# Kernel optimization log

Hardware: AMD Instinct MI355X
Metric: run time of the kernel (lower is better)

Reference implementation:

```python
import jax, jax.numpy as jnp
import numpy as np

NUM_CLASSES = 64


def setup_inputs() -> dict:
    key = jax.random.key(0)
    k1, k2, k3, k4, k5 = jax.random.split(key, 5)
    N, D = 65536, 256
    return {
        "src_feat": jax.random.normal(k1, (N, D), dtype=jnp.float32),
        "trg_feat": jax.random.normal(k2, (N, D), dtype=jnp.float32),
        "src_label": jax.random.randint(k3, (N,), 0, NUM_CLASSES, dtype=jnp.int64),
        "trg_label": jax.random.randint(k4, (N,), 0, NUM_CLASSES, dtype=jnp.int64),
        "trg_feat_un": jax.random.normal(k5, (N, D), dtype=jnp.float32),
    }


def _kl_mean(p_logits, q_logits):
    # torch F.kl_div(log_softmax(p), softmax(q), reduction='mean')
    # = mean over ALL elements of q * (log q - log_softmax(p))
    q = jax.nn.softmax(q_logits, axis=-1)
    logq = jax.nn.log_softmax(q_logits, axis=-1)
    logp = jax.nn.log_softmax(p_logits, axis=-1)
    return jnp.mean(q * (logq - logp))


def reference(src_feat, trg_feat, src_label, trg_label, trg_feat_un):
    C = NUM_CLASSES
    ones_s = jnp.ones(src_feat.shape[0], dtype=src_feat.dtype)
    ones_t = jnp.ones(trg_feat.shape[0], dtype=trg_feat.dtype)
    sum_s = jax.ops.segment_sum(src_feat, src_label, num_segments=C)  # [C,D]
    sum_t = jax.ops.segment_sum(trg_feat, trg_label, num_segments=C)  # [C,D]
    cnt_s = jax.ops.segment_sum(ones_s, src_label, num_segments=C)    # [C]
    cnt_t = jax.ops.segment_sum(ones_t, trg_label, num_segments=C)    # [C]
    u_s = sum_s / cnt_s[:, None]
    u_t = sum_t / cnt_t[:, None]
    u_st = (sum_s + sum_t) / (cnt_s + cnt_t)[:, None]

    feats = jnp.concatenate((src_feat, trg_feat), axis=0)  # [2N, D]
    P_s = feats @ u_s.T    # [2N, C]
    P_t = feats @ u_t.T
    P_st = feats @ u_st.T

    loss_st = (_kl_mean(P_s, P_t) + _kl_mean(P_t, P_s)) / 2
    loss_sst = (_kl_mean(P_s, P_st) + _kl_mean(P_st, P_s)) / 2
    loss_tst = (_kl_mean(P_t, P_st) + _kl_mean(P_st, P_t)) / 2
    return (loss_st + loss_sst + loss_tst) / 3
```

## Files before the change

### kernel.cpp

```cpp
#include <hip/hip_runtime.h>

#define N_ROWS 65536
#define DIMS 256
#define NCLS 64

#define P_SUM_S 0
#define P_SUM_T 131072
#define P_CNT_S 262144
#define P_CNT_T 262656
#define F_SUM_S 263168
#define F_SUM_T 279552
#define ACC_OFF 296064
#define BPACK_OFF 296080

typedef __attribute__((ext_vector_type(8))) short bf16x8;
typedef __attribute__((ext_vector_type(4))) float f32x4;

__device__ __forceinline__ short f2bf(float f) {
  unsigned u = __float_as_uint(f);
  u += 0x7fffu + ((u >> 16) & 1u);
  return (short)(u >> 16);
}

__device__ __forceinline__ float wave_sum64(float v) {
#pragma unroll
  for (int m = 32; m > 0; m >>= 1) v += __shfl_xor(v, m, 64);
  return v;
}
__device__ __forceinline__ float seg_max16(float v) {
#pragma unroll
  for (int m = 8; m > 0; m >>= 1) v = fmaxf(v, __shfl_xor(v, m, 64));
  return v;
}
__device__ __forceinline__ float seg_sum16(float v) {
#pragma unroll
  for (int m = 8; m > 0; m >>= 1) v += __shfl_xor(v, m, 64);
  return v;
}

__global__ __launch_bounds__(256) void seg_sum_kernel(
    const float* __restrict__ src_feat, const float* __restrict__ trg_feat,
    const int* __restrict__ src_label, const int* __restrict__ trg_label,
    float* __restrict__ ws_f) {
  __shared__ float lsum[NCLS * DIMS];
  const int tid = threadIdx.x;
  const bool is_trg = blockIdx.x >= 256;
  const int blk = is_trg ? (blockIdx.x - 256) : blockIdx.x;
  const int part = blockIdx.x & 7;
  const float* feat = is_trg ? trg_feat : src_feat;
  const int* label = is_trg ? trg_label : src_label;
  float* gsum = ws_f + (is_trg ? P_SUM_T : P_SUM_S) + part * 16384;
  float* gcnt = ws_f + (is_trg ? P_CNT_T : P_CNT_S) + part * 64;

  for (int i = tid; i < NCLS * DIMS; i += 256) lsum[i] = 0.f;
  __syncthreads();

  const int row0 = blk * 256;
  float cnt_local = 0.f;
  for (int r = 0; r < 256; r += 8) {
    int lb[8];
    float v[8];
#pragma unroll
    for (int i = 0; i < 8; ++i) {
      lb[i] = label[row0 + r + i];
      v[i] = feat[(size_t)(row0 + r + i) * DIMS + tid];
    }
#pragma unroll
    for (int i = 0; i < 8; ++i) {
      lsum[lb[i] * DIMS + tid] += v[i];
      if (tid < NCLS) cnt_local += (lb[i] == tid) ? 1.f : 0.f;
    }
  }
  __syncthreads();
  for (int c = 0; c < NCLS; ++c)
    atomicAdd(&gsum[c * DIMS + tid], lsum[c * DIMS + tid]);
  if (tid < NCLS) atomicAdd(&gcnt[tid], cnt_local);
}

__global__ __launch_bounds__(256) void reduce_kernel(float* __restrict__ ws_f) {
  const int i = blockIdx.x * 256 + threadIdx.x;
  const int which = i >> 14;
  const int off = i & 16383;
  const float* pp = ws_f + (which ? P_SUM_T : P_SUM_S) + off;
  float s = 0.f;
#pragma unroll
  for (int p = 0; p < 8; ++p) s += pp[p * 16384];
  ws_f[(which ? F_SUM_T : F_SUM_S) + off] = s;
}

__global__ __launch_bounds__(64) void pack_kernel(float* __restrict__ ws_f) {
  const int bx = blockIdx.x;
  const int mat = bx >> 2;
  const int tile = bx & 3;
  const int lane = threadIdx.x;
  const int c = tile * 16 + (lane & 15);

  float cs = 0.f, ct = 0.f;
#pragma unroll
  for (int p = 0; p < 8; ++p) {
    cs += ws_f[P_CNT_S + p * 64 + c];
    ct += ws_f[P_CNT_T + p * 64 + c];
  }

  bf16x8* out = (bf16x8*)(ws_f + BPACK_OFF);
  const float* ss_base = ws_f + F_SUM_S + c * DIMS;
  const float* st_base = ws_f + F_SUM_T + c * DIMS;

#pragma unroll
  for (int s = 0; s < 8; ++s) {
    const int k0 = s * 32 + (lane >> 4) * 8;
    bf16x8 v;
#pragma unroll
    for (int j = 0; j < 8; ++j) {
      const float ss = ss_base[k0 + j];
      const float st = st_base[k0 + j];
      float u;
      if (mat == 0) u = ss / cs;
      else if (mat == 1) u = st / ct;
      else u = (ss + st) / (cs + ct);
      v[j] = f2bf(u);
    }
    out[(bx * 8 + s) * 64 + lane] = v;
  }
}

__global__ __launch_bounds__(256, 2) void main_kernel(
    const float* __restrict__ src_feat, const float* __restrict__ trg_feat,
    const float* __restrict__ ws_f, double* __restrict__ acc_out) {
  const int tid = threadIdx.x;
  const int wave = tid >> 6;
  const int lane = tid & 63;
  const int row0 = blockIdx.x * 128 + wave * 32;
  const float* base = (row0 < N_ROWS)
                          ? src_feat + (size_t)row0 * DIMS
                          : trg_feat + (size_t)(row0 - N_ROWS) * DIMS;
  const float* ap = base + (size_t)((lane & 15) * DIMS + (lane >> 4) * 8);
  const bf16x8* bp = (const bf16x8*)(ws_f + BPACK_OFF);

  f32x4 C[3][4][2];
#pragma unroll
  for (int m = 0; m < 3; ++m)
#pragma unroll
    for (int t = 0; t < 4; ++t)
#pragma unroll
      for (int g = 0; g < 2; ++g) C[m][t][g] = (f32x4){0.f, 0.f, 0.f, 0.f};

#pragma unroll
  for (int s = 0; s < 8; ++s) {
    bf16x8 a[2];
#pragma unroll
    for (int g = 0; g < 2; ++g) {
      const float* p = ap + g * 16 * DIMS + s * 32;
      const float4 lo = *(const float4*)p;
      const float4 hi = *(const float4*)(p + 4);
      bf16x8 t;
      t[0] = f2bf(lo.x); t[1] = f2bf(lo.y); t[2] = f2bf(lo.z); t[3] = f2bf(lo.w);
      t[4] = f2bf(hi.x); t[5] = f2bf(hi.y); t[6] = f2bf(hi.z); t[7] = f2bf(hi.w);
      a[g] = t;
    }
#pragma unroll
    for (int mt = 0; mt < 12; ++mt) {
      const bf16x8 b = bp[(mt * 8 + s) * 64 + lane];
      C[mt >> 2][mt & 3][0] =
          __builtin_amdgcn_mfma_f32_16x16x32_bf16(a[0], b, C[mt >> 2][mt & 3][0], 0, 0, 0);
      C[mt >> 2][mt & 3][1] =
          __builtin_amdgcn_mfma_f32_16x16x32_bf16(a[1], b, C[mt >> 2][mt & 3][1], 0, 0, 0);
    }
  }

  float total = 0.f;
#pragma unroll
  for (int g = 0; g < 2; ++g) {
#pragma unroll
    for (int r = 0; r < 4; ++r) {
      float va[4], vb[4], vc[4];
#pragma unroll
      for (int t = 0; t < 4; ++t) {
        va[t] = C[0][t][g][r];
        vb[t] = C[1][t][g][r];
        vc[t] = C[2][t][g][r];
      }
      float ma = fmaxf(fmaxf(va[0], va[1]), fmaxf(va[2], va[3]));
      float mb = fmaxf(fmaxf(vb[0], vb[1]), fmaxf(vb[2], vb[3]));
      float mc = fmaxf(fmaxf(vc[0], vc[1]), fmaxf(vc[2], vc[3]));
      ma = seg_max16(ma); mb = seg_max16(mb); mc = seg_max16(mc);
      float ea[4], eb[4], ec[4];
      float sa = 0.f, sb = 0.f, sc = 0.f;
#pragma unroll
      for (int t = 0; t < 4; ++t) {
        ea[t] = __expf(va[t] - ma); sa += ea[t];
        eb[t] = __expf(vb[t] - mb); sb += eb[t];
        ec[t] = __expf(vc[t] - mc); sc += ec[t];
      }
      sa = seg_sum16(sa); sb = seg_sum16(sb); sc = seg_sum16(sc);
      const float La = ma + __logf(sa);
      const float Lb = mb + __logf(sb);
      const float Lc = mc + __logf(sc);
      const float isa = 1.f / sa, isb = 1.f / sb, isc = 1.f / sc;
#pragma unroll
      for (int t = 0; t < 4; ++t) {
        const float la = va[t] - La, lb = vb[t] - Lb, lc = vc[t] - Lc;
        const float pa = ea[t] * isa, pb = eb[t] * isb, pc = ec[t] * isc;
        total += pa * ((la - lb) + (la - lc)) + pb * ((lb - la) + (lb - lc)) +
                 pc * ((lc - la) + (lc - lb));
      }
    }
  }
  total = wave_sum64(total);
  if (lane == 0) atomicAdd(acc_out, (double)total);
}

__global__ void finalize_kernel(const double* __restrict__ acc,
                                float* __restrict__ out) {
  out[0] = (float)(acc[0] / 50331648.0);
}

extern "C" void kernel_launch(void* const* d_in, const int* in_sizes, int n_in,
                              void* d_out, int out_size, void* d_ws, size_t ws_size,
                              hipStream_t stream) {
  const float* src_feat = (const float*)d_in[0];
  const float* trg_feat = (const float*)d_in[1];
  const int* src_label = (const int*)d_in[2];
  const int* trg_label = (const int*)d_in[3];
  float* ws_f = (float*)d_ws;
  double* acc = (double*)(ws_f + ACC_OFF);
  float* out = (float*)d_out;

  hipMemsetAsync(d_ws, 0, (size_t)(P_CNT_T + 512) * sizeof(float), stream);
  hipMemsetAsync((void*)acc, 0, sizeof(double), stream);

  seg_sum_kernel<<<512, 256, 0, stream>>>(src_feat, trg_feat, src_label,
                                          trg_label, ws_f);
  reduce_kernel<<<128, 256, 0, stream>>>(ws_f);
  pack_kernel<<<12, 64, 0, stream>>>(ws_f);
  main_kernel<<<1024, 256, 0, stream>>>(src_feat, trg_feat, ws_f, acc);
  finalize_kernel<<<1, 1, 0, stream>>>(acc, out);
}
```

Measured before the change: 315.1 us.

## Factor class-mean scaling out of GEMM and stage bf16 features during segment sum

Computes only the two raw class-sum products per row (source and target sums) and gets the three logit sets by multiplying by per-class reciprocal counts. This drops one third of the MFMA work and one B matrix. The segment-sum pass also writes a bf16 copy of all features, which the main kernel reads instead of converting fp32. Other changes: the reduce kernel is folded into pack, finalize becomes a last-block-done atomic, and occupancy is raised to 4 blocks. The bf16 copy adds an extra global write of half the feature size in exchange for halving main-kernel reads, and rounding the raw sums to bf16 before scaling slightly changes numerics.

```diff
diff --git a/kernel.cpp b/kernel.cpp
--- a/kernel.cpp
+++ b/kernel.cpp
@@ -8,10 +8,12 @@
 #define P_SUM_T 131072
 #define P_CNT_S 262144
 #define P_CNT_T 262656
-#define F_SUM_S 263168
-#define F_SUM_T 279552
-#define ACC_OFF 296064
-#define BPACK_OFF 296080
+#define ACC_OFF 263168
+#define DONE_OFF 263170
+#define RECIP_OFF 263172
+#define BPACK_OFF 263424
+#define BF16A_OFF 279808
+#define ZERO_FLOATS 263172
 
 typedef __attribute__((ext_vector_type(8))) short bf16x8;
 typedef __attribute__((ext_vector_type(4))) float f32x4;
@@ -51,6 +53,8 @@
   const int* label = is_trg ? trg_label : src_label;
   float* gsum = ws_f + (is_trg ? P_SUM_T : P_SUM_S) + part * 16384;
   float* gcnt = ws_f + (is_trg ? P_CNT_T : P_CNT_S) + part * 64;
+  unsigned short* bfA = (unsigned short*)(ws_f + BF16A_OFF);
+  const size_t grow0 = (size_t)(is_trg ? N_ROWS : 0) + (size_t)blk * 256;
 
   for (int i = tid; i < NCLS * DIMS; i += 256) lsum[i] = 0.f;
   __syncthreads();
@@ -66,6 +70,9 @@
       v[i] = feat[(size_t)(row0 + r + i) * DIMS + tid];
     }
 #pragma unroll
+    for (int i = 0; i < 8; ++i)
+      bfA[(grow0 + r + i) * DIMS + tid] = (unsigned short)f2bf(v[i]);
+#pragma unroll
     for (int i = 0; i < 8; ++i) {
       lsum[lb[i] * DIMS + tid] += v[i];
       if (tid < NCLS) cnt_local += (lb[i] == tid) ? 1.f : 0.f;
@@ -75,17 +82,6 @@
   for (int c = 0; c < NCLS; ++c)
     atomicAdd(&gsum[c * DIMS + tid], lsum[c * DIMS + tid]);
   if (tid < NCLS) atomicAdd(&gcnt[tid], cnt_local);
-}
-
-__global__ __launch_bounds__(256) void reduce_kernel(float* __restrict__ ws_f) {
-  const int i = blockIdx.x * 256 + threadIdx.x;
-  const int which = i >> 14;
-  const int off = i & 16383;
-  const float* pp = ws_f + (which ? P_SUM_T : P_SUM_S) + off;
-  float s = 0.f;
-#pragma unroll
-  for (int p = 0; p < 8; ++p) s += pp[p * 16384];
-  ws_f[(which ? F_SUM_T : F_SUM_S) + off] = s;
 }
 
 __global__ __launch_bounds__(64) void pack_kernel(float* __restrict__ ws_f) {
@@ -101,45 +97,59 @@
     cs += ws_f[P_CNT_S + p * 64 + c];
     ct += ws_f[P_CNT_T + p * 64 + c];
   }
-
+  if (mat == 0 && lane < 16) {
+    ws_f[RECIP_OFF + c] = 1.f / cs;
+    ws_f[RECIP_OFF + 64 + c] = 1.f / ct;
+    ws_f[RECIP_OFF + 128 + c] = 1.f / (cs + ct);
+  }
+
+  const float* sb = ws_f + (mat ? P_SUM_T : P_SUM_S) + c * DIMS;
   bf16x8* out = (bf16x8*)(ws_f + BPACK_OFF);
-  const float* ss_base = ws_f + F_SUM_S + c * DIMS;
-  const float* st_base = ws_f + F_SUM_T + c * DIMS;
 
 #pragma unroll
   for (int s = 0; s < 8; ++s) {
     const int k0 = s * 32 + (lane >> 4) * 8;
+    float a8[8];
+#pragma unroll
+    for (int j = 0; j < 8; ++j) a8[j] = 0.f;
+#pragma unroll
+    for (int p = 0; p < 8; ++p) {
+      const float4 lo = *(const float4*)(sb + p * 16384 + k0);
+      const float4 hi = *(const float4*)(sb + p * 16384 + k0 + 4);
+      a8[0] += lo.x; a8[1] += lo.y; a8[2] += lo.z; a8[3] += lo.w;
+      a8[4] += hi.x; a8[5] += hi.y; a8[6] += hi.z; a8[7] += hi.w;
+    }
     bf16x8 v;
 #pragma unroll
-    for (int j = 0; j < 8; ++j) {
-      const float ss = ss_base[k0 + j];
-      const float st = st_base[k0 + j];
-      float u;
-      if (mat == 0) u = ss / cs;
-      else if (mat == 1) u = st / ct;
-      else u = (ss + st) / (cs + ct);
-      v[j] = f2bf(u);
-    }
-    out[(bx * 8 + s) * 64 + lane] = v;
-  }
-}
-
-__global__ __launch_bounds__(256, 2) void main_kernel(
-    const float* __restrict__ src_feat, const float* __restrict__ trg_feat,
-    const float* __restrict__ ws_f, double* __restrict__ acc_out) {
+    for (int j = 0; j < 8; ++j) v[j] = f2bf(a8[j]);
+    out[(s * 8 + bx) * 64 + lane] = v;
+  }
+}
+
+__global__ __launch_bounds__(256, 4) void main_kernel(
+    const float* __restrict__ ws_f, double* __restrict__ acc_out,
+    float* __restrict__ out) {
   const int tid = threadIdx.x;
   const int wave = tid >> 6;
   const int lane = tid & 63;
   const int row0 = blockIdx.x * 128 + wave * 32;
-  const float* base = (row0 < N_ROWS)
-                          ? src_feat + (size_t)row0 * DIMS
-                          : trg_feat + (size_t)(row0 - N_ROWS) * DIMS;
-  const float* ap = base + (size_t)((lane & 15) * DIMS + (lane >> 4) * 8);
+  const unsigned short* bfA = (const unsigned short*)(ws_f + BF16A_OFF);
+  const bf16x8* ap = (const bf16x8*)(bfA + (size_t)(row0 + (lane & 15)) * DIMS +
+                                     (lane >> 4) * 8);
   const bf16x8* bp = (const bf16x8*)(ws_f + BPACK_OFF);
 
-  f32x4 C[3][4][2];
-#pragma unroll
-  for (int m = 0; m < 3; ++m)
+  float rs[4], rt[4], rst[4];
+#pragma unroll
+  for (int t = 0; t < 4; ++t) {
+    const int c = t * 16 + (lane & 15);
+    rs[t] = ws_f[RECIP_OFF + c];
+    rt[t] = ws_f[RECIP_OFF + 64 + c];
+    rst[t] = ws_f[RECIP_OFF + 128 + c];
+  }
+
+  f32x4 C[2][4][2];
+#pragma unroll
+  for (int m = 0; m < 2; ++m)
 #pragma unroll
     for (int t = 0; t < 4; ++t)
 #pragma unroll
@@ -147,24 +157,15 @@
 
 #pragma unroll
   for (int s = 0; s < 8; ++s) {
-    bf16x8 a[2];
-#pragma unroll
-    for (int g = 0; g < 2; ++g) {
-      const float* p = ap + g * 16 * DIMS + s * 32;
-      const float4 lo = *(const float4*)p;
-      const float4 hi = *(const float4*)(p + 4);
-      bf16x8 t;
-      t[0] = f2bf(lo.x); t[1] = f2bf(lo.y); t[2] = f2bf(lo.z); t[3] = f2bf(lo.w);
-      t[4] = f2bf(hi.x); t[5] = f2bf(hi.y); t[6] = f2bf(hi.z); t[7] = f2bf(hi.w);
-      a[g] = t;
-    }
-#pragma unroll
-    for (int mt = 0; mt < 12; ++mt) {
-      const bf16x8 b = bp[(mt * 8 + s) * 64 + lane];
-      C[mt >> 2][mt & 3][0] =
-          __builtin_amdgcn_mfma_f32_16x16x32_bf16(a[0], b, C[mt >> 2][mt & 3][0], 0, 0, 0);
-      C[mt >> 2][mt & 3][1] =
-          __builtin_amdgcn_mfma_f32_16x16x32_bf16(a[1], b, C[mt >> 2][mt & 3][1], 0, 0, 0);
+    const bf16x8 a0 = ap[s * 4];
+    const bf16x8 a1 = ap[512 + s * 4];
+#pragma unroll
+    for (int mt = 0; mt < 8; ++mt) {
+      const bf16x8 b = bp[(s * 8 + mt) * 64 + lane];
+      C[mt >> 2][mt & 3][0] = __builtin_amdgcn_mfma_f32_16x16x32_bf16(
+          a0, b, C[mt >> 2][mt & 3][0], 0, 0, 0);
+      C[mt >> 2][mt & 3][1] = __builtin_amdgcn_mfma_f32_16x16x32_bf16(
+          a1, b, C[mt >> 2][mt & 3][1], 0, 0, 0);
     }
   }
 
@@ -176,9 +177,11 @@
       float va[4], vb[4], vc[4];
 #pragma unroll
       for (int t = 0; t < 4; ++t) {
-        va[t] = C[0][t][g][r];
-        vb[t] = C[1][t][g][r];
-        vc[t] = C[2][t][g][r];
+        const float gs = C[0][t][g][r];
+        const float gt = C[1][t][g][r];
+        va[t] = gs * rs[t];
+        vb[t] = gt * rt[t];
+        vc[t] = (gs + gt) * rst[t];
       }
       float ma = fmaxf(fmaxf(va[0], va[1]), fmaxf(va[2], va[3]));
       float mb = fmaxf(fmaxf(vb[0], vb[1]), fmaxf(vb[2], vb[3]));
@@ -208,11 +211,17 @@
   }
   total = wave_sum64(total);
   if (lane == 0) atomicAdd(acc_out, (double)total);
-}
-
-__global__ void finalize_kernel(const double* __restrict__ acc,
-                                float* __restrict__ out) {
-  out[0] = (float)(acc[0] / 50331648.0);
+
+  __syncthreads();
+  if (tid == 0) {
+    __threadfence();
+    unsigned* done = (unsigned*)(ws_f + DONE_OFF);
+    const unsigned old = atomicAdd(done, 1u);
+    if (old == gridDim.x - 1) {
+      const double a = atomicAdd(acc_out, 0.0);
+      out[0] = (float)(a / 50331648.0);
+    }
+  }
 }
 
 extern "C" void kernel_launch(void* const* d_in, const int* in_sizes, int n_in,
@@ -226,13 +235,10 @@
   double* acc = (double*)(ws_f + ACC_OFF);
   float* out = (float*)d_out;
 
-  hipMemsetAsync(d_ws, 0, (size_t)(P_CNT_T + 512) * sizeof(float), stream);
-  hipMemsetAsync((void*)acc, 0, sizeof(double), stream);
+  hipMemsetAsync(d_ws, 0, (size_t)ZERO_FLOATS * sizeof(float), stream);
 
   seg_sum_kernel<<<512, 256, 0, stream>>>(src_feat, trg_feat, src_label,
                                           trg_label, ws_f);
-  reduce_kernel<<<128, 256, 0, stream>>>(ws_f);
-  pack_kernel<<<12, 64, 0, stream>>>(ws_f);
-  main_kernel<<<1024, 256, 0, stream>>>(src_feat, trg_feat, ws_f, acc);
-  finalize_kernel<<<1, 1, 0, stream>>>(acc, out);
-}
+  pack_kernel<<<8, 64, 0, stream>>>(ws_f);
+  main_kernel<<<1024, 256, 0, stream>>>(ws_f, acc, out);
+}
```

After: 320.8 us. No clear change (+1.8%).
